# Performance work log

Hardware: AMD Instinct MI355X
Metric: run time of the kernel (lower is better)

## Reference

```python
import jax, jax.numpy as jnp
import numpy as np

PC_RANGE = [-51.2, -51.2, -5.0, 51.2, 51.2, 3.0]
VOXEL = [0.1, 0.1, 0.2]
OSF = 8
NUM_PRIOR = 100
C = 256
BN_EPS = 1e-5
LN_EPS = 1e-5


def _conv(x, w, pad):
    # x: [B,C,H,W], w: [O,I,kh,kw]
    return jax.lax.conv_general_dilated(
        x, w, window_strides=(1, 1), padding=[(pad, pad), (pad, pad)],
        dimension_numbers=('NCHW', 'OIHW', 'NCHW'))


def _bn(x, g, b, m, v):
    scale = (g / jnp.sqrt(v + BN_EPS))[None, :, None, None]
    return (x - m[None, :, None, None]) * scale + b[None, :, None, None]


def setup_inputs() -> dict:
    key = jax.random.key(0)
    ks = jax.random.split(key, 24)
    s3 = 1.0 / np.sqrt(C * 9)
    s1 = 1.0 / np.sqrt(C)
    inp = {
        'bev_feat': jax.random.normal(ks[0], (4, C, 128, 128), jnp.float32),
        'template_anchor': jax.random.normal(ks[1], (4, 900, 11), jnp.float32),
        # shared_conv: 3x3 conv (no bias) + BN(eval) + ReLU
        'shared_w': jax.random.normal(ks[2], (C, C, 3, 3), jnp.float32) * s3,
        'bn1_g': jax.random.normal(ks[3], (C,), jnp.float32) * 0.1 + 1.0,
        'bn1_b': jax.random.normal(ks[4], (C,), jnp.float32) * 0.1,
        'bn1_m': jax.random.normal(ks[5], (C,), jnp.float32) * 0.1,
        'bn1_v': jax.random.uniform(ks[6], (C,), jnp.float32) + 0.5,
        # objectness: 3x3 conv (no bias) + BN + ReLU + 1x1 conv (bias=-2)
        'obj_w1': jax.random.normal(ks[7], (C, C, 3, 3), jnp.float32) * s3,
        'bn2_g': jax.random.normal(ks[8], (C,), jnp.float32) * 0.1 + 1.0,
        'bn2_b': jax.random.normal(ks[9], (C,), jnp.float32) * 0.1,
        'bn2_m': jax.random.normal(ks[10], (C,), jnp.float32) * 0.1,
        'bn2_v': jax.random.uniform(ks[11], (C,), jnp.float32) + 0.5,
        'obj_w2': jax.random.normal(ks[12], (1, C, 1, 1), jnp.float32) * s1,
        'obj_b2': jnp.full((1,), -2.0, jnp.float32),
        # feat_proj: Linear + LN + ReLU + Linear
        'fp_w1': jax.random.normal(ks[13], (C, C), jnp.float32) * s1,
        'fp_b1': jax.random.normal(ks[14], (C,), jnp.float32) * 0.01,
        'ln_g': jnp.ones((C,), jnp.float32),
        'ln_b': jnp.zeros((C,), jnp.float32),
        'fp_w2': jax.random.normal(ks[15], (C, C), jnp.float32) * s1,
        'fp_b2': jax.random.normal(ks[16], (C,), jnp.float32) * 0.01,
        # geometry heads (1x1 convs, bias init 0)
        'z_w': jax.random.normal(ks[17], (1, C, 1, 1), jnp.float32) * s1,
        'z_b': jnp.zeros((1,), jnp.float32),
        'dim_w': jax.random.normal(ks[18], (3, C, 1, 1), jnp.float32) * s1,
        'dim_b': jnp.zeros((3,), jnp.float32),
        'yaw_w': jax.random.normal(ks[19], (2, C, 1, 1), jnp.float32) * s1,
        'yaw_b': jnp.zeros((2,), jnp.float32),
        'vel_w': jax.random.normal(ks[20], (2, C, 1, 1), jnp.float32) * s1,
        'vel_b': jnp.zeros((2,), jnp.float32),
    }
    return inp


def _forward(bev_feat, template_anchor, shared_w, bn1_g, bn1_b, bn1_m, bn1_v,
             obj_w1, bn2_g, bn2_b, bn2_m, bn2_v, obj_w2, obj_b2,
             fp_w1, fp_b1, ln_g, ln_b, fp_w2, fp_b2,
             z_w, z_b, dim_w, dim_b, yaw_w, yaw_b, vel_w, vel_b):
    B, Cc, H, W = bev_feat.shape
    # shared_conv
    feat = jax.nn.relu(_bn(_conv(bev_feat, shared_w, 1), bn1_g, bn1_b, bn1_m, bn1_v))
    # objectness heatmap
    h = jax.nn.relu(_bn(_conv(feat, obj_w1, 1), bn2_g, bn2_b, bn2_m, bn2_v))
    heatmap = jax.nn.sigmoid(_conv(h, obj_w2, 0) + obj_b2[None, :, None, None])
    score = heatmap.reshape(B, H * W)
    K = min(NUM_PRIOR, H * W, template_anchor.shape[1])
    topk_score, topk_inds = jax.lax.top_k(score, K)  # [B,K]
    ys = topk_inds // W
    xs = topk_inds % W
    # gather BEV features at topk locations: [B,K,C]
    feat_flat = feat.reshape(B, Cc, H * W).transpose(0, 2, 1)
    gathered = jnp.take_along_axis(feat_flat, topk_inds[:, :, None], axis=1)
    # feat_proj: Linear + LN + ReLU + Linear
    x = gathered @ fp_w1.T + fp_b1
    mu = jnp.mean(x, axis=-1, keepdims=True)
    var = jnp.mean((x - mu) ** 2, axis=-1, keepdims=True)
    x = (x - mu) / jnp.sqrt(var + LN_EPS) * ln_g + ln_b
    x = jax.nn.relu(x)
    prior_feature = x @ fp_w2.T + fp_b2
    prior_feature = prior_feature * (1.0 + topk_score[:, :, None])
    # geometry heads (1x1 convs == linear on gathered features)
    z_pred = gathered @ z_w[:, :, 0, 0].T + z_b      # [B,K,1]
    dim_pred = gathered @ dim_w[:, :, 0, 0].T + dim_b  # [B,K,3]
    yaw_pred = gathered @ yaw_w[:, :, 0, 0].T + yaw_b  # [B,K,2]
    vel_pred = gathered @ vel_w[:, :, 0, 0].T + vel_b  # [B,K,2]
    # anchor update
    pa = template_anchor[:, :K, :]
    x_metric = (xs.astype(pa.dtype) + 0.5) * (VOXEL[0] * OSF) + PC_RANGE[0]
    y_metric = (ys.astype(pa.dtype) + 0.5) * (VOXEL[1] * OSF) + PC_RANGE[1]
    z_new = pa[..., 2] + 0.5 * z_pred[..., 0]
    dims_new = pa[..., 3:6] + 0.2 * jnp.clip(dim_pred, -1.0, 1.0)
    yaw = jnp.tanh(yaw_pred)
    nrm = jnp.maximum(jnp.sqrt(jnp.sum(yaw * yaw, axis=-1, keepdims=True)), 1e-6)
    yaw_new = 0.7 * pa[..., 6:8] + 0.3 * (yaw / nrm)
    vel_new = pa[..., 8:10] + 0.2 * jnp.clip(vel_pred, -2.0, 2.0)
    prior_anchor = jnp.concatenate([
        x_metric[..., None], y_metric[..., None], z_new[..., None],
        dims_new, yaw_new, vel_new, pa[..., 10:]], axis=-1)
    return prior_feature, prior_anchor, topk_score


def reference(bev_feat, template_anchor, shared_w, bn1_g, bn1_b, bn1_m, bn1_v,
              obj_w1, bn2_g, bn2_b, bn2_m, bn2_v, obj_w2, obj_b2,
              fp_w1, fp_b1, ln_g, ln_b, fp_w2, fp_b2,
              z_w, z_b, dim_w, dim_b, yaw_w, yaw_b, vel_w, vel_b):
    return _forward(bev_feat, template_anchor, shared_w, bn1_g, bn1_b, bn1_m, bn1_v,
                    obj_w1, bn2_g, bn2_b, bn2_m, bn2_v, obj_w2, obj_b2,
                    fp_w1, fp_b1, ln_g, ln_b, fp_w2, fp_b2,
                    z_w, z_b, dim_w, dim_b, yaw_w, yaw_b, vel_w, vel_b)
```

## Files before the change

kernel.cpp:

```cpp
#include <hip/hip_runtime.h>
#include <math.h>


typedef __attribute__((ext_vector_type(8))) short bf16x8;
typedef __attribute__((ext_vector_type(4))) float f32x4;

#define HW 16384
#define WPITCH 130
#define CCAP 192
#define PSTR 28
#define WSO_XN    0ULL
#define WSO_FEATB 34078720ULL
#define WSO_WP1   68157440ULL
#define WSO_WP2   69337088ULL
#define WSO_BNP   70516736ULL
#define WSO_LOG   70521856ULL
#define WSO_CAND  70784000ULL
#define WSO_CNT   70787072ULL
#define WSO_EXL   70787136ULL
#define WSO_TIDX  70790208ULL
#define WSO_TLOG  70791808ULL
#define WSO_W1N   70793408ULL
#define WSO_W2N   73152704ULL
#define WSO_PBUF  WSO_XN

__device__ __forceinline__ float bf2f(short s) {
  return __uint_as_float(((unsigned)(unsigned short)s) << 16);
}
__device__ __forceinline__ short f2bf(float f) {
  unsigned u = __float_as_uint(f);
  u += 0x7fffu + ((u >> 16) & 1u);
  return (short)(u >> 16);
}
__device__ __forceinline__ void gll16(const void* g, void* l) {
  __builtin_amdgcn_global_load_lds(
      (const __attribute__((address_space(1))) void*)g,
      (__attribute__((address_space(3))) void*)l, 16, 0, 0);
}

__global__ void wprep2(const float* __restrict__ s1, const float* __restrict__ s2,
                       short* __restrict__ wp1, short* __restrict__ wp2,
                       float* __restrict__ wn1, float* __restrict__ wn2) {
  int bx = blockIdx.x;
  const float* src;
  short* wp;
  float* wn;
  if (bx >= 2304) {
    src = s2; wp = wp2; wn = wn2; bx -= 2304;
  } else {
    src = s1; wp = wp1; wn = wn1;
  }
  int i = bx * 256 + threadIdx.x;
  float v = src[i];
  int k = i % 9;
  int r = i / 9;
  int ci = r & 255;
  int co = r >> 8;
  wp[(k * 256 + co) * 256 + ci] = f2bf(v);
  wn[(ci * 9 + k) * 256 + co] = v;
}

__global__ void smallprep(const float* g1, const float* b1, const float* m1,
                          const float* v1, const float* g2, const float* b2,
                          const float* m2, const float* v2, const float* w2,
                          const float* ob2, float* __restrict__ bnp,
                          short* __restrict__ xn, short* __restrict__ featb,
                          float* __restrict__ logits) {
  const int blk = blockIdx.x, t = threadIdx.x;
  if (blk < 1024) {
    int i = blk * 256 + t;
    int c = i & 255;
    int r = i >> 8;
    int nh = r >> 1;
    int side = r & 1;
    size_t off = ((size_t)nh * WPITCH + (side ? 129 : 0)) * 256 + c;
    xn[off] = 0;
    featb[off] = 0;
  } else if (blk < 1280) {
    logits[(blk - 1024) * 256 + t] = ob2[0];
  } else {
    float s1 = g1[t] / sqrtf(v1[t] + 1e-5f);
    bnp[t] = s1;
    bnp[256 + t] = b1[t] - m1[t] * s1;
    float s2 = g2[t] / sqrtf(v2[t] + 1e-5f);
    bnp[512 + t] = s2;
    bnp[768 + t] = b2[t] - m2[t] * s2;
    bnp[1024 + t] = w2[t];
  }
}

__global__ __launch_bounds__(256) void nchw2nhwc(const float* __restrict__ in,
                                                 short* __restrict__ out) {
  __shared__ short tl[64 * 66];
  int n = blockIdx.z, c0 = blockIdx.y * 64, s0 = blockIdx.x * 64;
  int sl = threadIdx.x & 63, cl = threadIdx.x >> 6;
  for (int p = 0; p < 16; ++p) {
    int c = cl + p * 4;
    tl[c * 66 + sl] = f2bf(in[(((size_t)(n * 256 + c0 + c)) << 14) + s0 + sl]);
  }
  __syncthreads();
  int co = threadIdx.x & 63, so = threadIdx.x >> 6;
  for (int p = 0; p < 16; ++p) {
    int S = s0 + so + p * 4;
    int h = S >> 7, w = S & 127;
    out[(((size_t)(n * 128 + h)) * WPITCH + w + 1) * 256 + c0 + co] =
        tl[co * 66 + (so + p * 4)];
  }
}

template <int OUT_LOGITS>
__global__ __launch_bounds__(256) void conv3x3(const short* __restrict__ inp,
                                               const short* __restrict__ wp,
                                               const float* __restrict__ scale,
                                               const float* __restrict__ shift,
                                               const float* __restrict__ w2f,
                                               short* __restrict__ outb,
                                               float* __restrict__ logits) {
  __shared__ short a_sm[132 * 32];
  __shared__ short b_sm[3][128 * 32];
  const int t = threadIdx.x;
  const int wv = t >> 6, lane = t & 63;
  const int l15 = lane & 15, quad = lane >> 4;
  const int tile = blockIdx.x;
  const int img = tile >> 7;
  const int h = tile & 127;
  const int nblk = blockIdx.y;
  const int m0 = (wv & 1) << 6;
  const int n0 = (wv >> 1) << 6;

  f32x4 acc[4][4];
#pragma unroll
  for (int i = 0; i < 4; ++i)
#pragma unroll
    for (int j = 0; j < 4; ++j) {
      acc[i][j][0] = 0.f; acc[i][j][1] = 0.f;
      acc[i][j][2] = 0.f; acc[i][j][3] = 0.f;
    }

  for (int dhi = 0; dhi < 3; ++dhi) {
    const int hy = h + dhi - 1;
    if (hy < 0 || hy > 127) continue;
    const size_t arow = ((size_t)(img * 128 + hy)) * WPITCH;
    const short* wbase = wp + ((size_t)(dhi * 3 * 256 + nblk * 128)) * 256;

    for (int c0 = 0; c0 < 256; c0 += 32) {
      __syncthreads();
#pragma unroll
      for (int j = 0; j < 2; ++j) {
        const int seg = (j << 6) + (t >> 2);
        const int cc = t & 3;
        gll16(inp + (arow + seg) * 256 + c0 + cc * 8,
              a_sm + ((size_t)((j << 8) + t)) * 8);
      }
      if (t < 32) {
        const int r = t >> 4, dw = t & 15;
        const int* gsrc = (const int*)(inp + (arow + 128 + r) * 256 + c0) + dw;
        ((int*)a_sm)[(128 + r) * 16 + dw] = *gsrc;
      }
#pragma unroll
      for (int dwi = 0; dwi < 3; ++dwi) {
        const short* wtap = wbase + (size_t)dwi * 65536;
#pragma unroll
        for (int j = 0; j < 2; ++j) {
          const int nrow = (j << 6) + (t >> 2);
          const int cc = t & 3;
          gll16(wtap + (size_t)nrow * 256 + c0 + cc * 8,
                b_sm[dwi] + ((size_t)((j << 8) + t)) * 8);
        }
      }
      __syncthreads();

#pragma unroll
      for (int dwi = 0; dwi < 3; ++dwi) {
        bf16x8 af[4], bfr[4];
#pragma unroll
        for (int i = 0; i < 4; ++i)
          af[i] = *(const bf16x8*)(a_sm + (dwi + m0 + i * 16 + l15) * 32 + quad * 8);
#pragma unroll
        for (int i = 0; i < 4; ++i)
          bfr[i] = *(const bf16x8*)(b_sm[dwi] + (n0 + i * 16 + l15) * 32 + quad * 8);
#pragma unroll
        for (int i = 0; i < 4; ++i)
#pragma unroll
          for (int j = 0; j < 4; ++j)
            acc[i][j] = __builtin_amdgcn_mfma_f32_16x16x32_bf16(af[i], bfr[j],
                                                                acc[i][j], 0, 0, 0);
      }
    }
  }

  float sc[4], sh[4], wf[4];
#pragma unroll
  for (int j = 0; j < 4; ++j) {
    const int co = nblk * 128 + n0 + j * 16 + l15;
    sc[j] = scale[co];
    sh[j] = shift[co];
    if (OUT_LOGITS) wf[j] = w2f[co];
  }
  if (OUT_LOGITS) {
    float* lrow = logits + ((size_t)img << 14) + (h << 7);
#pragma unroll
    for (int i = 0; i < 4; ++i) {
#pragma unroll
      for (int r = 0; r < 4; ++r) {
        float part = 0.f;
#pragma unroll
        for (int j = 0; j < 4; ++j) {
          float v = fmaxf(acc[i][j][r] * sc[j] + sh[j], 0.f);
          part += v * wf[j];
        }
        part += __shfl_xor(part, 1);
        part += __shfl_xor(part, 2);
        part += __shfl_xor(part, 4);
        part += __shfl_xor(part, 8);
        if (l15 == 0)
          atomicAdd(&lrow[m0 + i * 16 + quad * 4 + r], part);
      }
    }
  } else {
    const size_t obase = ((size_t)(img * 128 + h)) * WPITCH + 1;
#pragma unroll
    for (int i = 0; i < 4; ++i) {
#pragma unroll
      for (int j = 0; j < 4; ++j) {
        const int co = nblk * 128 + n0 + j * 16 + l15;
#pragma unroll
        for (int r = 0; r < 4; ++r) {
          const int m = m0 + i * 16 + quad * 4 + r;
          float v = fmaxf(acc[i][j][r] * sc[j] + sh[j], 0.f);
          outb[(obase + m) * 256 + co] = f2bf(v);
        }
      }
    }
  }
}

__global__ __launch_bounds__(1024) void topk_radix(const float* __restrict__ logits,
                                                   int* __restrict__ cand,
                                                   int* __restrict__ cnt_out) {
  __shared__ int hist[2048];
  __shared__ int wsum[16];
  __shared__ unsigned sel_bin;
  __shared__ int sel_above;
  __shared__ int cntr;
  const int b = blockIdx.x, t = threadIdx.x;
  const int lane = t & 63, wid = t >> 6;
  const float* L = logits + (size_t)b * HW;
  const int base = t * 16;
  unsigned kv[16];
#pragma unroll
  for (int i = 0; i < 4; ++i) {
    float4 v = *(const float4*)(L + base + i * 4);
    float f4[4] = {v.x, v.y, v.z, v.w};
#pragma unroll
    for (int j = 0; j < 4; ++j) {
      unsigned u = __float_as_uint(f4[j]);
      kv[i * 4 + j] = u ^ (((unsigned)((int)u >> 31)) | 0x80000000u);
    }
  }
  unsigned prefix = 0, pmask = 0;
  int need = 128;
  const int shifts[3] = {21, 10, 0};
  const int nbs[3] = {2048, 2048, 1024};

  for (int lev = 0; lev < 3; ++lev) {
    const int shift = shifts[lev];
    const int nb = nbs[lev];
    hist[t] = 0;
    hist[t + 1024] = 0;
    __syncthreads();
#pragma unroll
    for (int i = 0; i < 16; ++i)
      if ((kv[i] & pmask) == prefix)
        atomicAdd(&hist[(kv[i] >> shift) & (nb - 1)], 1);
    __syncthreads();
    const int cs = nb >> 10;
    const int bin_hi = nb - 1 - t * cs;
    const int c_hi = hist[bin_hi];
    const int c_lo = (cs == 2) ? hist[bin_hi - 1] : 0;
    const int s = c_hi + c_lo;
    int inc = s;
    for (int off = 1; off < 64; off <<= 1) {
      int nbr = __shfl_up(inc, off);
      if (lane >= off) inc += nbr;
    }
    if (lane == 63) wsum[wid] = inc;
    __syncthreads();
    if (wid == 0) {
      int wv = (lane < 16) ? wsum[lane] : 0;
      for (int off = 1; off < 16; off <<= 1) {
        int nbr = __shfl_up(wv, off);
        if (lane >= off) wv += nbr;
      }
      if (lane < 16) wsum[lane] = wv;
    }
    __syncthreads();
    const int excl = inc - s + (wid ? wsum[wid - 1] : 0);
    if (excl < need && need <= excl + s) {
      if (need <= excl + c_hi) {
        sel_bin = (unsigned)bin_hi;
        sel_above = excl;
      } else {
        sel_bin = (unsigned)(bin_hi - 1);
        sel_above = excl + c_hi;
      }
    }
    __syncthreads();
    prefix |= sel_bin << shift;
    pmask |= ((unsigned)(nb - 1)) << shift;
    need -= sel_above;
    __syncthreads();
  }
  if (t == 0) cntr = 0;
  __syncthreads();
#pragma unroll
  for (int i = 0; i < 16; ++i) {
    if (kv[i] >= prefix) {
      int p = atomicAdd(&cntr, 1);
      if (p < CCAP) cand[b * CCAP + p] = base + i;
    }
  }
  __syncthreads();
  if (t == 0) cnt_out[b] = (cntr < CCAP) ? cntr : CCAP;
}

__global__ __launch_bounds__(256) void patchstage(const float* __restrict__ x,
                                                  const int* __restrict__ cand,
                                                  const int* __restrict__ cnt,
                                                  float* __restrict__ pbuf) {
  const int c = blockIdx.x, b = blockIdx.y, t = threadIdx.x;
  if (c >= cnt[b]) return;
  const int s = cand[b * CCAP + c];
  const int h0 = (s >> 7) - 2, w0 = (s & 127) - 2;
  const float* xb = x + ((size_t)b << 22);
  float* pc = pbuf + (size_t)(b * CCAP + c) * (256 * PSTR);
#pragma unroll
  for (int k = 0; k < 25; ++k) {
    int e = t + (k << 8);
    int ci = e / 25;
    int rj = e - ci * 25;
    int r = rj / 5;
    int j = rj - r * 5;
    int hy = h0 + r, wx = w0 + j;
    float v = 0.f;
    if (hy >= 0 && hy < 128 && wx >= 0 && wx < 128)
      v = xb[((size_t)ci << 14) + (hy << 7) + wx];
    pc[ci * PSTR + rj] = v;
  }
}

__global__ __launch_bounds__(1024) void rescore(const float* __restrict__ pbuf,
                                                const float* __restrict__ w1n,
                                                const float* __restrict__ w2n,
                                                const float* __restrict__ bnp,
                                                const float* __restrict__ b2,
                                                const int* __restrict__ cand,
                                                const int* __restrict__ cnt,
                                                float* __restrict__ exlog) {
  const int bx = blockIdx.x, b = blockIdx.y, t = threadIdx.x;
  const int n = cnt[b];
  const int co = t & 255;
  const int ks = __builtin_amdgcn_readfirstlane(t >> 8);
  const int ci0 = ks << 6;
  __shared__ float a1pA[4 * 256 * 9];
  __shared__ float a1pB[4 * 256 * 9];
  __shared__ float f9A[256 * 12];
  __shared__ float f9B[256 * 12];
  __shared__ float accA_p[4 * 256];
  __shared__ float accB_p[4 * 256];
  __shared__ float redA[4], redB[4];

  for (int pass = 0; pass < 2; ++pass) {
    const int c0 = bx + (pass ? 128 : 0);
    if (c0 >= n) break;
    const int c1 = bx + 64;
    const bool hasB = (pass == 0);
    if (pass) __syncthreads();

    const float* ppA = pbuf + ((size_t)(b * CCAP + c0)) * (256 * PSTR);
    const float* ppB = pbuf + ((size_t)(b * CCAP + (hasB ? c1 : c0))) * (256 * PSTR);

    float aA[9], aB[9];
#pragma unroll
    for (int p = 0; p < 9; ++p) { aA[p] = 0.f; aB[p] = 0.f; }
    for (int ci = ci0; ci < ci0 + 64; ++ci) {
      const float* wr = w1n + (size_t)ci * 2304 + co;
      float w9[9];
#pragma unroll
      for (int k = 0; k < 9; ++k) w9[k] = wr[k * 256];
      {
        const float* pc = ppA + ci * PSTR;
        float xp[25];
#pragma unroll
        for (int p = 0; p < 25; ++p) xp[p] = pc[p];
#pragma unroll
        for (int py = 0; py < 3; ++py)
#pragma unroll
          for (int px = 0; px < 3; ++px)
#pragma unroll
            for (int ky = 0; ky < 3; ++ky)
#pragma unroll
              for (int kx = 0; kx < 3; ++kx)
                aA[py * 3 + px] += w9[ky * 3 + kx] * xp[(py + ky) * 5 + px + kx];
      }
      if (hasB) {
        const float* pc = ppB + ci * PSTR;
        float xp[25];
#pragma unroll
        for (int p = 0; p < 25; ++p) xp[p] = pc[p];
#pragma unroll
        for (int py = 0; py < 3; ++py)
#pragma unroll
          for (int px = 0; px < 3; ++px)
#pragma unroll
            for (int ky = 0; ky < 3; ++ky)
#pragma unroll
              for (int kx = 0; kx < 3; ++kx)
                aB[py * 3 + px] += w9[ky * 3 + kx] * xp[(py + ky) * 5 + px + kx];
      }
    }
#pragma unroll
    for (int p = 0; p < 9; ++p) {
      a1pA[(ks * 256 + co) * 9 + p] = aA[p];
      if (hasB) a1pB[(ks * 256 + co) * 9 + p] = aB[p];
    }
    __syncthreads();

    if (t < 256) {
      const float sc1 = bnp[t], sh1 = bnp[256 + t];
#pragma unroll
      for (int p = 0; p < 9; ++p) {
        float vA = a1pA[t * 9 + p] + a1pA[(256 + t) * 9 + p] +
                   a1pA[(512 + t) * 9 + p] + a1pA[(768 + t) * 9 + p];
        f9A[t * 12 + p] = fmaxf(vA * sc1 + sh1, 0.f);
        if (hasB) {
          float vB = a1pB[t * 9 + p] + a1pB[(256 + t) * 9 + p] +
                     a1pB[(512 + t) * 9 + p] + a1pB[(768 + t) * 9 + p];
          f9B[t * 12 + p] = fmaxf(vB * sc1 + sh1, 0.f);
        }
      }
    }
    __syncthreads();

    float accA = 0.f, accB = 0.f;
    for (int ci = ci0; ci < ci0 + 64; ++ci) {
      const float* wr = w2n + (size_t)ci * 2304 + co;
      float w9[9];
#pragma unroll
      for (int k = 0; k < 9; ++k) w9[k] = wr[k * 256];
      {
        float f9[12];
        const float4* fr = (const float4*)(f9A + ci * 12);
#pragma unroll
        for (int q = 0; q < 3; ++q) {
          float4 v = fr[q];
          f9[q * 4 + 0] = v.x; f9[q * 4 + 1] = v.y;
          f9[q * 4 + 2] = v.z; f9[q * 4 + 3] = v.w;
        }
#pragma unroll
        for (int k = 0; k < 9; ++k) accA += w9[k] * f9[k];
      }
      if (hasB) {
        float f9[12];
        const float4* fr = (const float4*)(f9B + ci * 12);
#pragma unroll
        for (int q = 0; q < 3; ++q) {
          float4 v = fr[q];
          f9[q * 4 + 0] = v.x; f9[q * 4 + 1] = v.y;
          f9[q * 4 + 2] = v.z; f9[q * 4 + 3] = v.w;
        }
#pragma unroll
        for (int k = 0; k < 9; ++k) accB += w9[k] * f9[k];
      }
    }
    accA_p[ks * 256 + co] = accA;
    if (hasB) accB_p[ks * 256 + co] = accB;
    __syncthreads();

    if (t < 256) {
      const float sc2 = bnp[512 + t], sh2 = bnp[768 + t], wf = bnp[1024 + t];
      float a = accA_p[t] + accA_p[256 + t] + accA_p[512 + t] + accA_p[768 + t];
      float pA = fmaxf(a * sc2 + sh2, 0.f) * wf;
      float pB = 0.f;
      if (hasB) {
        float bb = accB_p[t] + accB_p[256 + t] + accB_p[512 + t] + accB_p[768 + t];
        pB = fmaxf(bb * sc2 + sh2, 0.f) * wf;
      }
      for (int off = 32; off; off >>= 1) {
        pA += __shfl_xor(pA, off);
        pB += __shfl_xor(pB, off);
      }
      if ((t & 63) == 0) {
        redA[t >> 6] = pA;
        redB[t >> 6] = pB;
      }
    }
    __syncthreads();
    if (t == 0) {
      exlog[b * CCAP + c0] = redA[0] + redA[1] + redA[2] + redA[3] + b2[0];
      if (hasB)
        exlog[b * CCAP + c1] = redB[0] + redB[1] + redB[2] + redB[3] + b2[0];
    }
  }
}

__global__ __launch_bounds__(CCAP) void final_topk(const float* __restrict__ exlog,
                                                   const int* __restrict__ cand,
                                                   const int* __restrict__ cnt,
                                                   int* __restrict__ tidx,
                                                   float* __restrict__ tlog) {
  const int b = blockIdx.x, t = threadIdx.x;
  __shared__ float v[CCAP];
  __shared__ int si[CCAP];
  const int n = cnt[b];
  float mv = (t < n) ? exlog[b * CCAP + t] : -3.0e38f;
  int s = (t < n) ? cand[b * CCAP + t] : 0x7FFFFFFF;
  v[t] = mv;
  si[t] = s;
  __syncthreads();
  int rank = 0;
  for (int j = 0; j < CCAP; ++j) {
    float vj = v[j];
    int sj = si[j];
    if (vj > mv || (vj == mv && sj < s)) ++rank;
  }
  if (t < n && rank < 100) {
    tidx[b * 100 + rank] = s;
    tlog[b * 100 + rank] = mv;
  }
}

__global__ __launch_bounds__(256) void head_kern(
    const short* __restrict__ featb, const int* __restrict__ tidx,
    const float* __restrict__ tlog, const float* __restrict__ tmpl,
    const float* __restrict__ w1, const float* __restrict__ b1,
    const float* __restrict__ lng, const float* __restrict__ lnb,
    const float* __restrict__ w2, const float* __restrict__ b2,
    const float* __restrict__ zw, const float* __restrict__ zb,
    const float* __restrict__ dmw, const float* __restrict__ dmb,
    const float* __restrict__ yw, const float* __restrict__ yb,
    const float* __restrict__ vw, const float* __restrict__ vb,
    float* __restrict__ out) {
  const int blk = blockIdx.x;
  const int b = blk / 100, q = blk % 100;
  const int t = threadIdx.x;
  const int lane = t & 63, wid = t >> 6;
  __shared__ float g[256];
  __shared__ float sx[256];
  __shared__ float red[4];
  __shared__ float heads[8];

  const int s = tidx[b * 100 + q];
  const float score = 1.f / (1.f + expf(-tlog[b * 100 + q]));
  const int ys = s >> 7, xs = s & 127;

  g[t] = bf2f(featb[(((size_t)(b * 128 + ys)) * WPITCH + xs + 1) * 256 + t]);
  __syncthreads();

  float x = b1[t];
  {
    const float* wr = w1 + (size_t)t * 256;
    for (int i = 0; i < 256; i += 4) {
      float4 wv = *(const float4*)(wr + i);
      x += g[i] * wv.x + g[i + 1] * wv.y + g[i + 2] * wv.z + g[i + 3] * wv.w;
    }
  }
  float sum = x;
  for (int off = 32; off; off >>= 1) sum += __shfl_xor(sum, off);
  if (lane == 0) red[wid] = sum;
  __syncthreads();
  float mu = (red[0] + red[1] + red[2] + red[3]) * (1.f / 256.f);
  __syncthreads();
  float d = x - mu;
  float q2 = d * d;
  for (int off = 32; off; off >>= 1) q2 += __shfl_xor(q2, off);
  if (lane == 0) red[wid] = q2;
  __syncthreads();
  float var = (red[0] + red[1] + red[2] + red[3]) * (1.f / 256.f);
  float xn = d * (1.f / sqrtf(var + 1e-5f)) * lng[t] + lnb[t];
  xn = fmaxf(xn, 0.f);
  sx[t] = xn;
  __syncthreads();
  float pf = b2[t];
  {
    const float* wr = w2 + (size_t)t * 256;
    for (int i = 0; i < 256; i += 4) {
      float4 wv = *(const float4*)(wr + i);
      pf += sx[i] * wv.x + sx[i + 1] * wv.y + sx[i + 2] * wv.z + sx[i + 3] * wv.w;
    }
  }
  pf *= (1.f + score);
  out[(size_t)(b * 100 + q) * 256 + t] = pf;

  const int k = t >> 5, l = t & 31;
  const float* hw;
  float hb;
  if (k == 0)      { hw = zw;                 hb = zb[0]; }
  else if (k < 4)  { hw = dmw + (k - 1) * 256; hb = dmb[k - 1]; }
  else if (k < 6)  { hw = yw + (k - 4) * 256;  hb = yb[k - 4]; }
  else             { hw = vw + (k - 6) * 256;  hb = vb[k - 6]; }
  float hp = 0.f;
#pragma unroll
  for (int r = 0; r < 8; ++r) {
    int i = l + r * 32;
    hp += g[i] * hw[i];
  }
  for (int off = 16; off; off >>= 1) hp += __shfl_xor(hp, off);
  if (l == 0) heads[k] = hp + hb;
  __syncthreads();

  if (t == 0) {
    const float* pa = tmpl + ((size_t)b * 900 + q) * 11;
    float p[11];
#pragma unroll
    for (int i = 0; i < 11; ++i) p[i] = pa[i];
    float a[11];
    a[0] = ((float)xs + 0.5f) * 0.8f - 51.2f;
    a[1] = ((float)ys + 0.5f) * 0.8f - 51.2f;
    a[2] = p[2] + 0.5f * heads[0];
#pragma unroll
    for (int i = 0; i < 3; ++i)
      a[3 + i] = p[3 + i] + 0.2f * fminf(fmaxf(heads[1 + i], -1.f), 1.f);
    float t0 = tanhf(heads[4]), t1 = tanhf(heads[5]);
    float nrm = fmaxf(sqrtf(t0 * t0 + t1 * t1), 1e-6f);
    a[6] = 0.7f * p[6] + 0.3f * t0 / nrm;
    a[7] = 0.7f * p[7] + 0.3f * t1 / nrm;
    a[8] = p[8] + 0.2f * fminf(fmaxf(heads[6], -2.f), 2.f);
    a[9] = p[9] + 0.2f * fminf(fmaxf(heads[7], -2.f), 2.f);
    a[10] = p[10];
    float* oa = out + 102400 + (size_t)(b * 100 + q) * 11;
#pragma unroll
    for (int i = 0; i < 11; ++i) oa[i] = a[i];
    out[106800 + b * 100 + q] = score;
  }
}

extern "C" void kernel_launch(void* const* d_in, const int* in_sizes, int n_in,
                              void* d_out, int out_size, void* d_ws, size_t ws_size,
                              hipStream_t stream) {
  (void)in_sizes; (void)n_in; (void)out_size; (void)ws_size;
  char* ws = (char*)d_ws;
  short* xn     = (short*)(ws + WSO_XN);
  short* featb  = (short*)(ws + WSO_FEATB);
  short* wp1    = (short*)(ws + WSO_WP1);
  short* wp2    = (short*)(ws + WSO_WP2);
  float* bnp    = (float*)(ws + WSO_BNP);
  float* logits = (float*)(ws + WSO_LOG);
  int*   cand   = (int*)(ws + WSO_CAND);
  int*   cnt    = (int*)(ws + WSO_CNT);
  float* exl    = (float*)(ws + WSO_EXL);
  int*   tidx   = (int*)(ws + WSO_TIDX);
  float* tlog   = (float*)(ws + WSO_TLOG);
  float* w1n    = (float*)(ws + WSO_W1N);
  float* w2n    = (float*)(ws + WSO_W2N);
  float* pbuf   = (float*)(ws + WSO_PBUF);

  const float* bev = (const float*)d_in[0];

  wprep2<<<4608, 256, 0, stream>>>((const float*)d_in[2], (const float*)d_in[7],
                                   wp1, wp2, w1n, w2n);
  smallprep<<<1281, 256, 0, stream>>>(
      (const float*)d_in[3], (const float*)d_in[4], (const float*)d_in[5],
      (const float*)d_in[6], (const float*)d_in[8], (const float*)d_in[9],
      (const float*)d_in[10], (const float*)d_in[11], (const float*)d_in[12],
      (const float*)d_in[13], bnp, xn, featb, logits);
  nchw2nhwc<<<dim3(256, 4, 4), 256, 0, stream>>>(bev, xn);
  conv3x3<0><<<dim3(512, 2), 256, 0, stream>>>(xn, wp1, bnp, bnp + 256,
                                               nullptr, featb, nullptr);
  conv3x3<1><<<dim3(512, 2), 256, 0, stream>>>(featb, wp2, bnp + 512, bnp + 768,
                                               bnp + 1024, nullptr, logits);
  topk_radix<<<4, 1024, 0, stream>>>(logits, cand, cnt);
  patchstage<<<dim3(CCAP, 4), 256, 0, stream>>>(bev, cand, cnt, pbuf);
  rescore<<<dim3(64, 4), 1024, 0, stream>>>(pbuf, w1n, w2n, bnp,
                                            (const float*)d_in[13], cand, cnt,
                                            exl);
  final_topk<<<4, CCAP, 0, stream>>>(exl, cand, cnt, tidx, tlog);
  head_kern<<<400, 256, 0, stream>>>(
      featb, tidx, tlog, (const float*)d_in[1],
      (const float*)d_in[14], (const float*)d_in[15], (const float*)d_in[16],
      (const float*)d_in[17], (const float*)d_in[18], (const float*)d_in[19],
      (const float*)d_in[20], (const float*)d_in[21], (const float*)d_in[22],
      (const float*)d_in[23], (const float*)d_in[24], (const float*)d_in[25],
      (const float*)d_in[26], (const float*)d_in[27], (float*)d_out);
}
```

Measured before the change: 552.0 us.

## Split rescore into patch-fused first conv and batched second conv kernels

Replaces the patch-staging kernel plus the monolithic 1024-thread rescore with two kernels. The first gathers each candidate pair's 5x5 patches straight from the BEV input into shared memory, computes partial first-conv sums per 64-channel slice, and writes them to global memory. The second reduces those partials, applies BN+ReLU, and runs the centre-tap second conv for 8 candidates per block so each weight load is reused across candidates. This removes the patch buffer round trip and spreads the work over many more blocks, at the cost of an extra launch and a global write/read of the partial sums.

```diff
diff --git a/kernel.cpp b/kernel.cpp
--- a/kernel.cpp
+++ b/kernel.cpp
@@ -22,7 +22,7 @@
 #define WSO_TLOG  70791808ULL
 #define WSO_W1N   70793408ULL
 #define WSO_W2N   73152704ULL
-#define WSO_PBUF  WSO_XN
+#define WSO_A1P   WSO_XN
 
 __device__ __forceinline__ float bf2f(short s) {
   return __uint_as_float(((unsigned)(unsigned short)s) << 16);
@@ -324,183 +324,186 @@
   if (t == 0) cnt_out[b] = (cntr < CCAP) ? cntr : CCAP;
 }
 
-__global__ __launch_bounds__(256) void patchstage(const float* __restrict__ x,
-                                                  const int* __restrict__ cand,
-                                                  const int* __restrict__ cnt,
-                                                  float* __restrict__ pbuf) {
-  const int c = blockIdx.x, b = blockIdx.y, t = threadIdx.x;
-  if (c >= cnt[b]) return;
-  const int s = cand[b * CCAP + c];
-  const int h0 = (s >> 7) - 2, w0 = (s & 127) - 2;
-  const float* xb = x + ((size_t)b << 22);
-  float* pc = pbuf + (size_t)(b * CCAP + c) * (256 * PSTR);
-#pragma unroll
-  for (int k = 0; k < 25; ++k) {
-    int e = t + (k << 8);
-    int ci = e / 25;
-    int rj = e - ci * 25;
-    int r = rj / 5;
-    int j = rj - r * 5;
-    int hy = h0 + r, wx = w0 + j;
-    float v = 0.f;
-    if (hy >= 0 && hy < 128 && wx >= 0 && wx < 128)
-      v = xb[((size_t)ci << 14) + (hy << 7) + wx];
-    pc[ci * PSTR + rj] = v;
-  }
-}
-
-__global__ __launch_bounds__(1024) void rescore(const float* __restrict__ pbuf,
-                                                const float* __restrict__ w1n,
-                                                const float* __restrict__ w2n,
-                                                const float* __restrict__ bnp,
-                                                const float* __restrict__ b2,
-                                                const int* __restrict__ cand,
-                                                const int* __restrict__ cnt,
-                                                float* __restrict__ exlog) {
+__global__ __launch_bounds__(256) void rescore_a(const float* __restrict__ bev,
+                                                 const float* __restrict__ w1n,
+                                                 const int* __restrict__ cand,
+                                                 const int* __restrict__ cnt,
+                                                 float* __restrict__ a1part) {
+  const int bx = blockIdx.x, b = blockIdx.y, z = blockIdx.z;
+  const int t = threadIdx.x;
+  const int n = cnt[b];
+  const int c0 = bx * 2;
+  if (c0 >= n) return;
+  const bool hasB = (c0 + 1 < n);
+  const int ci0 = z << 6;
+  __shared__ float patch[2 * 64 * PSTR];
+
+  {
+    const int TE = hasB ? 3200 : 1600;
+    const int s0 = cand[b * CCAP + c0];
+    const int s1 = hasB ? cand[b * CCAP + c0 + 1] : s0;
+#pragma unroll
+    for (int k = 0; k < 13; ++k) {
+      int e = t + (k << 8);
+      if (e < TE) {
+        int g = (e >= 1600) ? 1 : 0;
+        int rem = e - g * 1600;
+        int ci = rem / 25;
+        int rj = rem - ci * 25;
+        int r = rj / 5;
+        int j = rj - r * 5;
+        int s = g ? s1 : s0;
+        int hy = (s >> 7) - 2 + r, wx = (s & 127) - 2 + j;
+        float v = 0.f;
+        if (hy >= 0 && hy < 128 && wx >= 0 && wx < 128)
+          v = bev[(((size_t)(b * 256 + ci0 + ci)) << 14) + (hy << 7) + wx];
+        patch[(g * 64 + ci) * PSTR + rj] = v;
+      }
+    }
+  }
+  __syncthreads();
+
+  const int co = t;
+  float aA[9], aB[9];
+#pragma unroll
+  for (int p = 0; p < 9; ++p) { aA[p] = 0.f; aB[p] = 0.f; }
+
+  for (int ci = 0; ci < 64; ++ci) {
+    const float* wr = w1n + (size_t)(ci0 + ci) * 2304 + co;
+    float w9[9];
+#pragma unroll
+    for (int k = 0; k < 9; ++k) w9[k] = wr[k * 256];
+    {
+      const float4* pr = (const float4*)(patch + ci * PSTR);
+      float xp[28];
+#pragma unroll
+      for (int q = 0; q < 7; ++q) {
+        float4 v = pr[q];
+        xp[q * 4 + 0] = v.x; xp[q * 4 + 1] = v.y;
+        xp[q * 4 + 2] = v.z; xp[q * 4 + 3] = v.w;
+      }
+#pragma unroll
+      for (int py = 0; py < 3; ++py)
+#pragma unroll
+        for (int px = 0; px < 3; ++px)
+#pragma unroll
+          for (int ky = 0; ky < 3; ++ky)
+#pragma unroll
+            for (int kx = 0; kx < 3; ++kx)
+              aA[py * 3 + px] += w9[ky * 3 + kx] * xp[(py + ky) * 5 + px + kx];
+    }
+    if (hasB) {
+      const float4* pr = (const float4*)(patch + (64 + ci) * PSTR);
+      float xp[28];
+#pragma unroll
+      for (int q = 0; q < 7; ++q) {
+        float4 v = pr[q];
+        xp[q * 4 + 0] = v.x; xp[q * 4 + 1] = v.y;
+        xp[q * 4 + 2] = v.z; xp[q * 4 + 3] = v.w;
+      }
+#pragma unroll
+      for (int py = 0; py < 3; ++py)
+#pragma unroll
+        for (int px = 0; px < 3; ++px)
+#pragma unroll
+          for (int ky = 0; ky < 3; ++ky)
+#pragma unroll
+            for (int kx = 0; kx < 3; ++kx)
+              aB[py * 3 + px] += w9[ky * 3 + kx] * xp[(py + ky) * 5 + px + kx];
+    }
+  }
+
+  float* dstA = a1part + ((((size_t)(b * CCAP + c0) * 4 + z) * 9) << 8) + co;
+#pragma unroll
+  for (int p = 0; p < 9; ++p) dstA[p << 8] = aA[p];
+  if (hasB) {
+    float* dstB = a1part + ((((size_t)(b * CCAP + c0 + 1) * 4 + z) * 9) << 8) + co;
+#pragma unroll
+    for (int p = 0; p < 9; ++p) dstB[p << 8] = aB[p];
+  }
+}
+
+__global__ __launch_bounds__(256) void rescore_b(const float* __restrict__ a1part,
+                                                 const float* __restrict__ w2n,
+                                                 const float* __restrict__ bnp,
+                                                 const float* __restrict__ b2,
+                                                 const int* __restrict__ cnt,
+                                                 float* __restrict__ exlog) {
   const int bx = blockIdx.x, b = blockIdx.y, t = threadIdx.x;
   const int n = cnt[b];
-  const int co = t & 255;
-  const int ks = __builtin_amdgcn_readfirstlane(t >> 8);
-  const int ci0 = ks << 6;
-  __shared__ float a1pA[4 * 256 * 9];
-  __shared__ float a1pB[4 * 256 * 9];
-  __shared__ float f9A[256 * 12];
-  __shared__ float f9B[256 * 12];
-  __shared__ float accA_p[4 * 256];
-  __shared__ float accB_p[4 * 256];
-  __shared__ float redA[4], redB[4];
-
-  for (int pass = 0; pass < 2; ++pass) {
-    const int c0 = bx + (pass ? 128 : 0);
-    if (c0 >= n) break;
-    const int c1 = bx + 64;
-    const bool hasB = (pass == 0);
-    if (pass) __syncthreads();
-
-    const float* ppA = pbuf + ((size_t)(b * CCAP + c0)) * (256 * PSTR);
-    const float* ppB = pbuf + ((size_t)(b * CCAP + (hasB ? c1 : c0))) * (256 * PSTR);
-
-    float aA[9], aB[9];
-#pragma unroll
-    for (int p = 0; p < 9; ++p) { aA[p] = 0.f; aB[p] = 0.f; }
-    for (int ci = ci0; ci < ci0 + 64; ++ci) {
-      const float* wr = w1n + (size_t)ci * 2304 + co;
-      float w9[9];
-#pragma unroll
-      for (int k = 0; k < 9; ++k) w9[k] = wr[k * 256];
-      {
-        const float* pc = ppA + ci * PSTR;
-        float xp[25];
-#pragma unroll
-        for (int p = 0; p < 25; ++p) xp[p] = pc[p];
-#pragma unroll
-        for (int py = 0; py < 3; ++py)
-#pragma unroll
-          for (int px = 0; px < 3; ++px)
-#pragma unroll
-            for (int ky = 0; ky < 3; ++ky)
-#pragma unroll
-              for (int kx = 0; kx < 3; ++kx)
-                aA[py * 3 + px] += w9[ky * 3 + kx] * xp[(py + ky) * 5 + px + kx];
-      }
-      if (hasB) {
-        const float* pc = ppB + ci * PSTR;
-        float xp[25];
-#pragma unroll
-        for (int p = 0; p < 25; ++p) xp[p] = pc[p];
-#pragma unroll
-        for (int py = 0; py < 3; ++py)
-#pragma unroll
-          for (int px = 0; px < 3; ++px)
-#pragma unroll
-            for (int ky = 0; ky < 3; ++ky)
-#pragma unroll
-              for (int kx = 0; kx < 3; ++kx)
-                aB[py * 3 + px] += w9[ky * 3 + kx] * xp[(py + ky) * 5 + px + kx];
-      }
-    }
-#pragma unroll
-    for (int p = 0; p < 9; ++p) {
-      a1pA[(ks * 256 + co) * 9 + p] = aA[p];
-      if (hasB) a1pB[(ks * 256 + co) * 9 + p] = aB[p];
-    }
-    __syncthreads();
-
-    if (t < 256) {
-      const float sc1 = bnp[t], sh1 = bnp[256 + t];
-#pragma unroll
-      for (int p = 0; p < 9; ++p) {
-        float vA = a1pA[t * 9 + p] + a1pA[(256 + t) * 9 + p] +
-                   a1pA[(512 + t) * 9 + p] + a1pA[(768 + t) * 9 + p];
-        f9A[t * 12 + p] = fmaxf(vA * sc1 + sh1, 0.f);
-        if (hasB) {
-          float vB = a1pB[t * 9 + p] + a1pB[(256 + t) * 9 + p] +
-                     a1pB[(512 + t) * 9 + p] + a1pB[(768 + t) * 9 + p];
-          f9B[t * 12 + p] = fmaxf(vB * sc1 + sh1, 0.f);
-        }
-      }
-    }
-    __syncthreads();
-
-    float accA = 0.f, accB = 0.f;
-    for (int ci = ci0; ci < ci0 + 64; ++ci) {
-      const float* wr = w2n + (size_t)ci * 2304 + co;
-      float w9[9];
-#pragma unroll
-      for (int k = 0; k < 9; ++k) w9[k] = wr[k * 256];
-      {
-        float f9[12];
-        const float4* fr = (const float4*)(f9A + ci * 12);
-#pragma unroll
-        for (int q = 0; q < 3; ++q) {
-          float4 v = fr[q];
-          f9[q * 4 + 0] = v.x; f9[q * 4 + 1] = v.y;
-          f9[q * 4 + 2] = v.z; f9[q * 4 + 3] = v.w;
-        }
-#pragma unroll
-        for (int k = 0; k < 9; ++k) accA += w9[k] * f9[k];
-      }
-      if (hasB) {
-        float f9[12];
-        const float4* fr = (const float4*)(f9B + ci * 12);
-#pragma unroll
-        for (int q = 0; q < 3; ++q) {
-          float4 v = fr[q];
-          f9[q * 4 + 0] = v.x; f9[q * 4 + 1] = v.y;
-          f9[q * 4 + 2] = v.z; f9[q * 4 + 3] = v.w;
-        }
-#pragma unroll
-        for (int k = 0; k < 9; ++k) accB += w9[k] * f9[k];
-      }
-    }
-    accA_p[ks * 256 + co] = accA;
-    if (hasB) accB_p[ks * 256 + co] = accB;
-    __syncthreads();
-
-    if (t < 256) {
-      const float sc2 = bnp[512 + t], sh2 = bnp[768 + t], wf = bnp[1024 + t];
-      float a = accA_p[t] + accA_p[256 + t] + accA_p[512 + t] + accA_p[768 + t];
-      float pA = fmaxf(a * sc2 + sh2, 0.f) * wf;
-      float pB = 0.f;
-      if (hasB) {
-        float bb = accB_p[t] + accB_p[256 + t] + accB_p[512 + t] + accB_p[768 + t];
-        pB = fmaxf(bb * sc2 + sh2, 0.f) * wf;
-      }
-      for (int off = 32; off; off >>= 1) {
-        pA += __shfl_xor(pA, off);
-        pB += __shfl_xor(pB, off);
-      }
-      if ((t & 63) == 0) {
-        redA[t >> 6] = pA;
-        redB[t >> 6] = pB;
-      }
-    }
-    __syncthreads();
-    if (t == 0) {
-      exlog[b * CCAP + c0] = redA[0] + redA[1] + redA[2] + redA[3] + b2[0];
-      if (hasB)
-        exlog[b * CCAP + c1] = redB[0] + redB[1] + redB[2] + redB[3] + b2[0];
-    }
+  const int cbase = bx * 8;
+  if (cbase >= n) return;
+  __shared__ float f9[8 * 256 * 12];
+  __shared__ float red[4][8];
+
+  const float sc1 = bnp[t], sh1 = bnp[256 + t];
+#pragma unroll
+  for (int g = 0; g < 8; ++g) {
+    const int c = cbase + g;
+    if (c < n) {
+      const float* src = a1part + (((size_t)(b * CCAP + c) * 4) * 9 << 8) + t;
+      float a[9];
+#pragma unroll
+      for (int p = 0; p < 9; ++p) a[p] = 0.f;
+#pragma unroll
+      for (int half = 0; half < 4; ++half) {
+        const float* s2 = src + (((size_t)half * 9) << 8);
+#pragma unroll
+        for (int p = 0; p < 9; ++p) a[p] += s2[p << 8];
+      }
+#pragma unroll
+      for (int p = 0; p < 9; ++p)
+        f9[(g * 256 + t) * 12 + p] = fmaxf(a[p] * sc1 + sh1, 0.f);
+    } else {
+#pragma unroll
+      for (int p = 0; p < 9; ++p) f9[(g * 256 + t) * 12 + p] = 0.f;
+    }
+  }
+  __syncthreads();
+
+  float acc[8];
+#pragma unroll
+  for (int g = 0; g < 8; ++g) acc[g] = 0.f;
+  for (int ci = 0; ci < 256; ++ci) {
+    const float* wr = w2n + (size_t)ci * 2304 + t;
+    float w9[9];
+#pragma unroll
+    for (int k = 0; k < 9; ++k) w9[k] = wr[k * 256];
+#pragma unroll
+    for (int g = 0; g < 8; ++g) {
+      const float4* fp = (const float4*)(f9 + (g * 256 + ci) * 12);
+      float4 f0 = fp[0], f1 = fp[1], f2 = fp[2];
+      acc[g] += w9[0] * f0.x;
+      acc[g] += w9[1] * f0.y;
+      acc[g] += w9[2] * f0.z;
+      acc[g] += w9[3] * f0.w;
+      acc[g] += w9[4] * f1.x;
+      acc[g] += w9[5] * f1.y;
+      acc[g] += w9[6] * f1.z;
+      acc[g] += w9[7] * f1.w;
+      acc[g] += w9[8] * f2.x;
+    }
+  }
+
+  const float sc2 = bnp[512 + t], sh2 = bnp[768 + t], wf = bnp[1024 + t];
+  float pg[8];
+#pragma unroll
+  for (int g = 0; g < 8; ++g)
+    pg[g] = fmaxf(acc[g] * sc2 + sh2, 0.f) * wf;
+#pragma unroll
+  for (int off = 32; off; off >>= 1)
+#pragma unroll
+    for (int g = 0; g < 8; ++g) pg[g] += __shfl_xor(pg[g], off);
+  const int lane = t & 63, wid = t >> 6;
+  if (lane == 0)
+#pragma unroll
+    for (int g = 0; g < 8; ++g) red[wid][g] = pg[g];
+  __syncthreads();
+  if (t < 8) {
+    const int c = cbase + t;
+    if (c < n)
+      exlog[b * CCAP + c] =
+          red[0][t] + red[1][t] + red[2][t] + red[3][t] + b2[0];
   }
 }
 
@@ -653,7 +656,7 @@
   float* tlog   = (float*)(ws + WSO_TLOG);
   float* w1n    = (float*)(ws + WSO_W1N);
   float* w2n    = (float*)(ws + WSO_W2N);
-  float* pbuf   = (float*)(ws + WSO_PBUF);
+  float* a1p    = (float*)(ws + WSO_A1P);
 
   const float* bev = (const float*)d_in[0];
 
@@ -670,10 +673,10 @@
   conv3x3<1><<<dim3(512, 2), 256, 0, stream>>>(featb, wp2, bnp + 512, bnp + 768,
                                                bnp + 1024, nullptr, logits);
   topk_radix<<<4, 1024, 0, stream>>>(logits, cand, cnt);
-  patchstage<<<dim3(CCAP, 4), 256, 0, stream>>>(bev, cand, cnt, pbuf);
-  rescore<<<dim3(64, 4), 1024, 0, stream>>>(pbuf, w1n, w2n, bnp,
-                                            (const float*)d_in[13], cand, cnt,
-                                            exl);
+  rescore_a<<<dim3(CCAP / 2, 4, 4), 256, 0, stream>>>(bev, w1n, cand, cnt, a1p);
+  rescore_b<<<dim3(CCAP / 8, 4), 256, 0, stream>>>(a1p, w2n, bnp,
+                                                   (const float*)d_in[13], cnt,
+                                                   exl);
   final_topk<<<4, CCAP, 0, stream>>>(exl, cand, cnt, tidx, tlog);
   head_kern<<<400, 256, 0, stream>>>(
       featb, tidx, tlog, (const float*)d_in[1],
```

After: 635.6 us. +15.2%, slower.
